# Optimization experiments

Hardware: AMD Instinct MI355X
Metric: run time of the kernel (lower is better)

Reference implementation:

```python
import jax, jax.numpy as jnp
import numpy as np

N = 50000      # nodes
E = 800000     # edges (before self-loops)
IN = 256       # input features
H = 8          # heads
C = 32         # hidden channels per head
OUT = 40       # classes
NEG_SLOPE = 0.2


def setup_inputs() -> dict:
    key = jax.random.key(0)
    ks = jax.random.split(key, 12)
    sd = lambda k, sh: (jax.random.normal(k, sh, jnp.float32) * 0.05)
    return {
        "x": jax.random.normal(ks[0], (N, IN), jnp.float32),
        "edge_index": jax.random.randint(ks[1], (2, E), 0, N),
        "W1": sd(ks[2], (IN, H * C)),
        "a_src1": sd(ks[3], (H, C)),
        "a_dst1": sd(ks[4], (H, C)),
        "b1": jnp.zeros((C,), jnp.float32),
        "W2": sd(ks[5], (C, H * C)),
        "a_src2": sd(ks[6], (H, C)),
        "a_dst2": sd(ks[7], (H, C)),
        "b2": jnp.zeros((C,), jnp.float32),
        "Wo": sd(ks[8], (C, OUT)),
        "bo": jnp.zeros((OUT,), jnp.float32),
    }


def gat_layer(x, src, dst, n, W, a_src, a_dst, b):
    # x: [N, F]; src/dst: [E'] (self-loops included). concat=False -> mean over heads.
    h = (x @ W).reshape(n, H, C)                       # [N, H, C]
    alpha_src = jnp.sum(h * a_src, axis=-1)            # [N, H]
    alpha_dst = jnp.sum(h * a_dst, axis=-1)            # [N, H]
    e = alpha_src[src] + alpha_dst[dst]                # [E', H]
    e = jnp.where(e > 0, e, NEG_SLOPE * e)             # leaky_relu
    # segment softmax over incoming edges of each dst node
    m = jax.ops.segment_max(e, dst, num_segments=n)    # [N, H]
    ex = jnp.exp(e - m[dst])                           # [E', H]
    s = jax.ops.segment_sum(ex, dst, num_segments=n)   # [N, H]
    alpha = ex / s[dst]                                # [E', H]
    msg = alpha[:, :, None] * h[src]                   # [E', H, C]
    out = jax.ops.segment_sum(msg, dst, num_segments=n)  # [N, H, C]
    return out.mean(axis=1) + b                        # [N, C]


def reference(x, edge_index, W1, a_src1, a_dst1, b1, W2, a_src2, a_dst2, b2, Wo, bo):
    n = x.shape[0]
    loops = jnp.arange(n, dtype=edge_index.dtype)
    src = jnp.concatenate([edge_index[0], loops])      # add self-loops (PyG default)
    dst = jnp.concatenate([edge_index[1], loops])
    h = gat_layer(x, src, dst, n, W1, a_src1, a_dst1, b1)
    h = jax.nn.elu(h)                                  # dropout skipped (eval)
    h = gat_layer(h, src, dst, n, W2, a_src2, a_dst2, b2)
    h = jax.nn.elu(h)
    logits = h @ Wo + bo
    return jax.nn.log_softmax(logits, axis=1)
```

## Files before the change

kernel.cpp:

```cpp
#include <hip/hip_runtime.h>
#include <math.h>

#define N_NODES 50000
#define N_PAD   50016
#define N_EDGES 800000
#define E_TOT   (N_EDGES + N_NODES)
#define F_IN    256
#define NHEAD   8
#define CH      32
#define HC      256
#define OUT_C   40
#define NEG_SLOPE 0.2f
#define SCAN_BLOCKS ((N_NODES + 255) / 256)
#define G_DEG   ((E_TOT + 255) / 256)
#define G_XCVT  ((N_NODES * F_IN / 8 + 255) / 256)
#define G_WCVT  ((HC * F_IN + 255) / 256)
#define G_WCVT2 ((HC * CH + 255) / 256)

typedef unsigned short u16;
typedef unsigned int   u32;
typedef unsigned char  u8;
typedef __attribute__((ext_vector_type(8))) short bf16x8;
typedef __attribute__((ext_vector_type(4))) float f32x4;
typedef __attribute__((ext_vector_type(2))) float f32x2;

__device__ __forceinline__ u16 f2bf(float f) {
    union { u32 u; float f; } x; x.f = f;
    u32 u = x.u;
    return (u16)((u + 0x7fffu + ((u >> 16) & 1u)) >> 16);
}
__device__ __forceinline__ float bflo(u32 v) {
    union { u32 u; float f; } x; x.u = v << 16; return x.f;
}
__device__ __forceinline__ u8 f2fp8(float f) {
    return (u8)(__builtin_amdgcn_cvt_pk_fp8_f32(f, f, 0, false) & 0xff);
}


__global__ __launch_bounds__(256) void cvt_kernel(const float* __restrict__ x,
        u16* __restrict__ xb, const float* __restrict__ W1, u16* __restrict__ Wt,
        const float* __restrict__ W2, u16* __restrict__ W2t,
        const int* __restrict__ ei, int* __restrict__ deg) {
    int b = blockIdx.x;
    if (b < G_DEG) {
        int j = b * 256 + threadIdx.x;
        if (j >= E_TOT) return;
        int dstn = (j < N_EDGES) ? ei[N_EDGES + j] : (j - N_EDGES);
        atomicAdd(&deg[dstn], 1);
    } else if (b < G_DEG + G_XCVT) {
        int t = (b - G_DEG) * 256 + threadIdx.x;
        if (t >= N_NODES * F_IN / 8) return;
        const float4* xp = (const float4*)x + (size_t)t * 2;
        float4 v0 = xp[0], v1 = xp[1];
        uint4 o;
        o.x = (u32)f2bf(v0.x) | ((u32)f2bf(v0.y) << 16);
        o.y = (u32)f2bf(v0.z) | ((u32)f2bf(v0.w) << 16);
        o.z = (u32)f2bf(v1.x) | ((u32)f2bf(v1.y) << 16);
        o.w = (u32)f2bf(v1.z) | ((u32)f2bf(v1.w) << 16);
        ((uint4*)xb)[t] = o;
    } else if (b < G_DEG + G_XCVT + G_WCVT) {
        int t = (b - G_DEG - G_XCVT) * 256 + threadIdx.x;
        int n = t & 255, k = t >> 8;
        Wt[(size_t)n * F_IN + k] = f2bf(W1[(size_t)k * HC + n]);
    } else {
        int t = (b - G_DEG - G_XCVT - G_WCVT) * 256 + threadIdx.x;
        if (t >= HC * CH) return;
        int n = t & 255, k = t >> 8;
        W2t[(size_t)n * CH + k] = f2bf(W2[(size_t)k * HC + n]);
    }
}

__global__ __launch_bounds__(256) void gemm1_mfma(const u16* __restrict__ xb,
        const u16* __restrict__ Wt, u8* __restrict__ ht8) {
    const int row0 = blockIdx.x * 32;
    const int t    = threadIdx.x;
    const int wave = t >> 6;
    const int lane = t & 63;
    const int l16  = lane & 15;
    const int quad = lane >> 4;
    const int nb   = wave * 64;

    f32x4 acc[2][4];
    #pragma unroll
    for (int m = 0; m < 2; ++m)
        #pragma unroll
        for (int n = 0; n < 4; ++n) acc[m][n] = (f32x4){0.f, 0.f, 0.f, 0.f};

    const u16* a0p = xb + (size_t)(row0 + l16) * F_IN;
    const u16* a1p = a0p + 16 * F_IN;
    const u16* bp  = Wt + (size_t)(nb + l16) * F_IN;

    #pragma unroll 1
    for (int k0 = 0; k0 < F_IN; k0 += 32) {
        const int ko = k0 + quad * 8;
        bf16x8 a0 = *(const bf16x8*)(a0p + ko);
        bf16x8 a1 = *(const bf16x8*)(a1p + ko);
        bf16x8 b0 = *(const bf16x8*)(bp + 0 * 16 * F_IN + ko);
        bf16x8 b1 = *(const bf16x8*)(bp + 1 * 16 * F_IN + ko);
        bf16x8 b2 = *(const bf16x8*)(bp + 2 * 16 * F_IN + ko);
        bf16x8 b3 = *(const bf16x8*)(bp + 3 * 16 * F_IN + ko);
        acc[0][0] = __builtin_amdgcn_mfma_f32_16x16x32_bf16(a0, b0, acc[0][0], 0, 0, 0);
        acc[0][1] = __builtin_amdgcn_mfma_f32_16x16x32_bf16(a0, b1, acc[0][1], 0, 0, 0);
        acc[0][2] = __builtin_amdgcn_mfma_f32_16x16x32_bf16(a0, b2, acc[0][2], 0, 0, 0);
        acc[0][3] = __builtin_amdgcn_mfma_f32_16x16x32_bf16(a0, b3, acc[0][3], 0, 0, 0);
        acc[1][0] = __builtin_amdgcn_mfma_f32_16x16x32_bf16(a1, b0, acc[1][0], 0, 0, 0);
        acc[1][1] = __builtin_amdgcn_mfma_f32_16x16x32_bf16(a1, b1, acc[1][1], 0, 0, 0);
        acc[1][2] = __builtin_amdgcn_mfma_f32_16x16x32_bf16(a1, b2, acc[1][2], 0, 0, 0);
        acc[1][3] = __builtin_amdgcn_mfma_f32_16x16x32_bf16(a1, b3, acc[1][3], 0, 0, 0);
    }

    #pragma unroll
    for (int m = 0; m < 2; ++m) {
        #pragma unroll
        for (int r = 0; r < 4; ++r) {
            int row = row0 + m * 16 + quad * 4 + r;
            if (row < N_NODES) {
                u8* hr = ht8 + (size_t)row * HC;
                #pragma unroll
                for (int n = 0; n < 4; ++n) {
                    int col = nb + n * 16 + l16;
                    hr[col] = f2fp8(acc[m][n][r]);
                }
            }
        }
    }
}

__global__ __launch_bounds__(256) void gemm2_mfma(const u16* __restrict__ hmb,
        const u16* __restrict__ W2t, u8* __restrict__ ht8) {
    const int row0 = blockIdx.x * 32;
    const int t    = threadIdx.x;
    const int wave = t >> 6;
    const int lane = t & 63;
    const int l16  = lane & 15;
    const int quad = lane >> 4;
    const int nb   = wave * 64;
    const int ko   = quad * 8;

    const u16* a0p = hmb + (size_t)(row0 + l16) * CH;
    const u16* a1p = a0p + 16 * CH;
    const u16* bp  = W2t + (size_t)(nb + l16) * CH;

    bf16x8 a0 = *(const bf16x8*)(a0p + ko);
    bf16x8 a1 = *(const bf16x8*)(a1p + ko);
    bf16x8 b0 = *(const bf16x8*)(bp + 0 * 16 * CH + ko);
    bf16x8 b1 = *(const bf16x8*)(bp + 1 * 16 * CH + ko);
    bf16x8 b2 = *(const bf16x8*)(bp + 2 * 16 * CH + ko);
    bf16x8 b3 = *(const bf16x8*)(bp + 3 * 16 * CH + ko);

    f32x4 z = (f32x4){0.f, 0.f, 0.f, 0.f};
    f32x4 acc[2][4];
    acc[0][0] = __builtin_amdgcn_mfma_f32_16x16x32_bf16(a0, b0, z, 0, 0, 0);
    acc[0][1] = __builtin_amdgcn_mfma_f32_16x16x32_bf16(a0, b1, z, 0, 0, 0);
    acc[0][2] = __builtin_amdgcn_mfma_f32_16x16x32_bf16(a0, b2, z, 0, 0, 0);
    acc[0][3] = __builtin_amdgcn_mfma_f32_16x16x32_bf16(a0, b3, z, 0, 0, 0);
    acc[1][0] = __builtin_amdgcn_mfma_f32_16x16x32_bf16(a1, b0, z, 0, 0, 0);
    acc[1][1] = __builtin_amdgcn_mfma_f32_16x16x32_bf16(a1, b1, z, 0, 0, 0);
    acc[1][2] = __builtin_amdgcn_mfma_f32_16x16x32_bf16(a1, b2, z, 0, 0, 0);
    acc[1][3] = __builtin_amdgcn_mfma_f32_16x16x32_bf16(a1, b3, z, 0, 0, 0);

    #pragma unroll
    for (int m = 0; m < 2; ++m) {
        #pragma unroll
        for (int r = 0; r < 4; ++r) {
            int row = row0 + m * 16 + quad * 4 + r;
            if (row < N_NODES) {
                u8* hr = ht8 + (size_t)row * HC;
                #pragma unroll
                for (int n = 0; n < 4; ++n) {
                    int col = nb + n * 16 + l16;
                    hr[col] = f2fp8(acc[m][n][r]);
                }
            }
        }
    }
}

__global__ __launch_bounds__(256) void alpha_t_kernel(const u8* __restrict__ ht8,
        const float* __restrict__ a_src, const float* __restrict__ a_dst,
        float* __restrict__ asrc, float* __restrict__ adst) {
    __shared__ float sas[HC], sad[HC];
    for (int i = threadIdx.x; i < HC; i += 256) {
        sas[i] = a_src[i];
        sad[i] = a_dst[i];
    }
    __syncthreads();
    int node = blockIdx.x * 256 + threadIdx.x;
    if (node >= N_NODES) return;
    const uint2* hp = (const uint2*)(ht8 + (size_t)node * HC);
    float s1[NHEAD], s2[NHEAD];
    #pragma unroll
    for (int h = 0; h < NHEAD; ++h) {
        float t1 = 0.f, t2 = 0.f;
        #pragma unroll
        for (int i = 0; i < 4; ++i) {
            uint2 v = hp[h * 4 + i];
            f32x2 p01 = __builtin_amdgcn_cvt_pk_f32_fp8(v.x, false);
            f32x2 p23 = __builtin_amdgcn_cvt_pk_f32_fp8(v.x, true);
            f32x2 p45 = __builtin_amdgcn_cvt_pk_f32_fp8(v.y, false);
            f32x2 p67 = __builtin_amdgcn_cvt_pk_f32_fp8(v.y, true);
            const float* s1p = &sas[h * CH + i * 8];
            const float* s2p = &sad[h * CH + i * 8];
            t1 += p01.x * s1p[0] + p01.y * s1p[1] + p23.x * s1p[2] + p23.y * s1p[3]
                + p45.x * s1p[4] + p45.y * s1p[5] + p67.x * s1p[6] + p67.y * s1p[7];
            t2 += p01.x * s2p[0] + p01.y * s2p[1] + p23.x * s2p[2] + p23.y * s2p[3]
                + p45.x * s2p[4] + p45.y * s2p[5] + p67.x * s2p[6] + p67.y * s2p[7];
        }
        s1[h] = t1; s2[h] = t2;
    }
    float4* o1 = (float4*)(asrc + (size_t)node * NHEAD);
    float4* o2 = (float4*)(adst + (size_t)node * NHEAD);
    o1[0] = make_float4(s1[0], s1[1], s1[2], s1[3]);
    o1[1] = make_float4(s1[4], s1[5], s1[6], s1[7]);
    o2[0] = make_float4(s2[0], s2[1], s2[2], s2[3]);
    o2[1] = make_float4(s2[4], s2[5], s2[6], s2[7]);
}

__device__ __forceinline__ int wave_incl_scan(int v, int lane) {
    #pragma unroll
    for (int d = 1; d < 64; d <<= 1) {
        int u = __shfl_up(v, d, 64);
        if (lane >= d) v += u;
    }
    return v;
}

__global__ __launch_bounds__(256) void scan1_kernel(const int* __restrict__ deg,
        int* __restrict__ rowptr, int* __restrict__ partials) {
    const int t    = blockIdx.x * 256 + threadIdx.x;
    const int lane = threadIdx.x & 63;
    const int wid  = threadIdx.x >> 6;
    int v = (t < N_NODES) ? deg[t] : 0;
    int inc = wave_incl_scan(v, lane);
    __shared__ int wtot[4];
    if (lane == 63) wtot[wid] = inc;
    __syncthreads();
    int woff = 0;
    #pragma unroll
    for (int i = 0; i < 4; ++i) woff += (i < wid) ? wtot[i] : 0;
    if (t < N_NODES) rowptr[t] = inc - v + woff;
    if (threadIdx.x == 255) partials[blockIdx.x] = woff + inc;
}

__global__ __launch_bounds__(256) void scan2_kernel(int* __restrict__ partials) {
    const int t    = threadIdx.x;
    const int lane = t & 63;
    const int wid  = t >> 6;
    int v = (t < SCAN_BLOCKS) ? partials[t] : 0;
    int inc = wave_incl_scan(v, lane);
    __shared__ int wtot[4];
    if (lane == 63) wtot[wid] = inc;
    __syncthreads();
    int woff = 0;
    #pragma unroll
    for (int i = 0; i < 4; ++i) woff += (i < wid) ? wtot[i] : 0;
    __syncthreads();
    if (t < SCAN_BLOCKS) partials[t] = inc - v + woff;
}

__global__ __launch_bounds__(256) void scan3_kernel(int* __restrict__ rowptr,
        int* __restrict__ cursor, const int* __restrict__ partials) {
    const int t = blockIdx.x * 256 + threadIdx.x;
    if (t < N_NODES) {
        int v = rowptr[t] + partials[blockIdx.x];
        rowptr[t] = v;
        cursor[t] = v;
    } else if (t == N_NODES) {
        rowptr[N_NODES] = E_TOT;
    }
}

__global__ __launch_bounds__(256) void scatter_kernel(const int* __restrict__ ei,
        int* __restrict__ cursor, u16* __restrict__ csr_src) {
    int j = blockIdx.x * 256 + threadIdx.x;
    if (j >= E_TOT) return;
    int src, dst;
    if (j < N_EDGES) { src = ei[j]; dst = ei[N_EDGES + j]; }
    else             { src = j - N_EDGES; dst = src; }
    int pos = atomicAdd(&cursor[dst], 1);
    csr_src[pos] = (u16)src;
}

__global__ __launch_bounds__(256) void attn_kernel(const int* __restrict__ rowptr,
        const u16* __restrict__ csr_src, const float* __restrict__ asrc,
        const float* __restrict__ adst, const u8* __restrict__ ht8,
        const float* __restrict__ b, u16* __restrict__ out) {
    const int wid = (blockIdx.x * 256 + threadIdx.x) >> 6;
    if (wid >= N_NODES) return;
    const int dst  = wid;
    const int lane = threadIdx.x & 63;
    const int q    = lane >> 4;
    const int l16  = lane & 15;
    const int h    = l16 >> 1;
    const float ad_own = adst[dst * NHEAD + h];
    const u8* hbase = ht8 + l16 * 16;

    f32x2 acc2[8];
    #pragma unroll
    for (int i = 0; i < 8; ++i) acc2[i] = (f32x2){0.f, 0.f};
    float wsum = 0.f;

    const int p0 = rowptr[dst], p1 = rowptr[dst + 1];
    const int nt = (p1 - p0 + 7) >> 3;

    float asA = -1e30f, asB = -1e30f;
    uint4 hvA = make_uint4(0u, 0u, 0u, 0u), hvB = make_uint4(0u, 0u, 0u, 0u);
    int e = p0 + q;
    if (e < p1) {
        int s = (int)csr_src[e];
        asA = asrc[s * NHEAD + h];
        hvA = *(const uint4*)(hbase + ((size_t)s << 8));
    }
    if (e + 4 < p1) {
        int s = (int)csr_src[e + 4];
        asB = asrc[s * NHEAD + h];
        hvB = *(const uint4*)(hbase + ((size_t)s << 8));
    }

    for (int it = 0; it < nt; ++it) {
        float aA = asA; uint4 hA = hvA;
        float aB = asB; uint4 hB = hvB;
        asA = -1e30f; asB = -1e30f;
        if (e + 8 < p1) {
            int s = (int)csr_src[e + 8];
            asA = asrc[s * NHEAD + h];
            hvA = *(const uint4*)(hbase + ((size_t)s << 8));
        }
        if (e + 12 < p1) {
            int s = (int)csr_src[e + 12];
            asB = asrc[s * NHEAD + h];
            hvB = *(const uint4*)(hbase + ((size_t)s << 8));
        }
        {
            float x = aA + ad_own;
            x = x > 0.f ? x : NEG_SLOPE * x;
            float w = __expf(x);
            wsum += w;
            f32x2 w2; w2.x = w; w2.y = w;
            acc2[0] = __builtin_elementwise_fma(w2, __builtin_amdgcn_cvt_pk_f32_fp8(hA.x, false), acc2[0]);
            acc2[1] = __builtin_elementwise_fma(w2, __builtin_amdgcn_cvt_pk_f32_fp8(hA.x, true ), acc2[1]);
            acc2[2] = __builtin_elementwise_fma(w2, __builtin_amdgcn_cvt_pk_f32_fp8(hA.y, false), acc2[2]);
            acc2[3] = __builtin_elementwise_fma(w2, __builtin_amdgcn_cvt_pk_f32_fp8(hA.y, true ), acc2[3]);
            acc2[4] = __builtin_elementwise_fma(w2, __builtin_amdgcn_cvt_pk_f32_fp8(hA.z, false), acc2[4]);
            acc2[5] = __builtin_elementwise_fma(w2, __builtin_amdgcn_cvt_pk_f32_fp8(hA.z, true ), acc2[5]);
            acc2[6] = __builtin_elementwise_fma(w2, __builtin_amdgcn_cvt_pk_f32_fp8(hA.w, false), acc2[6]);
            acc2[7] = __builtin_elementwise_fma(w2, __builtin_amdgcn_cvt_pk_f32_fp8(hA.w, true ), acc2[7]);
        }
        {
            float x = aB + ad_own;
            x = x > 0.f ? x : NEG_SLOPE * x;
            float w = __expf(x);
            wsum += w;
            f32x2 w2; w2.x = w; w2.y = w;
            acc2[0] = __builtin_elementwise_fma(w2, __builtin_amdgcn_cvt_pk_f32_fp8(hB.x, false), acc2[0]);
            acc2[1] = __builtin_elementwise_fma(w2, __builtin_amdgcn_cvt_pk_f32_fp8(hB.x, true ), acc2[1]);
            acc2[2] = __builtin_elementwise_fma(w2, __builtin_amdgcn_cvt_pk_f32_fp8(hB.y, false), acc2[2]);
            acc2[3] = __builtin_elementwise_fma(w2, __builtin_amdgcn_cvt_pk_f32_fp8(hB.y, true ), acc2[3]);
            acc2[4] = __builtin_elementwise_fma(w2, __builtin_amdgcn_cvt_pk_f32_fp8(hB.z, false), acc2[4]);
            acc2[5] = __builtin_elementwise_fma(w2, __builtin_amdgcn_cvt_pk_f32_fp8(hB.z, true ), acc2[5]);
            acc2[6] = __builtin_elementwise_fma(w2, __builtin_amdgcn_cvt_pk_f32_fp8(hB.w, false), acc2[6]);
            acc2[7] = __builtin_elementwise_fma(w2, __builtin_amdgcn_cvt_pk_f32_fp8(hB.w, true ), acc2[7]);
        }
        e += 8;
    }

    #pragma unroll
    for (int i = 0; i < 8; ++i) {
        acc2[i].x += __shfl_xor(acc2[i].x, 16, 64);
        acc2[i].y += __shfl_xor(acc2[i].y, 16, 64);
        acc2[i].x += __shfl_xor(acc2[i].x, 32, 64);
        acc2[i].y += __shfl_xor(acc2[i].y, 32, 64);
    }
    wsum += __shfl_xor(wsum, 16, 64);
    wsum += __shfl_xor(wsum, 32, 64);

    float winv = 1.0f / wsum;
    f32x2 winv2; winv2.x = winv; winv2.y = winv;
    #pragma unroll
    for (int i = 0; i < 8; ++i) acc2[i] *= winv2;

    #pragma unroll
    for (int i = 0; i < 8; ++i) {
        acc2[i].x += __shfl_xor(acc2[i].x, 2, 64);
        acc2[i].y += __shfl_xor(acc2[i].y, 2, 64);
        acc2[i].x += __shfl_xor(acc2[i].x, 4, 64);
        acc2[i].y += __shfl_xor(acc2[i].y, 4, 64);
        acc2[i].x += __shfl_xor(acc2[i].x, 8, 64);
        acc2[i].y += __shfl_xor(acc2[i].y, 8, 64);
    }

    if (lane < 2) {
        const int c0 = lane * 16;
        const float4* bp4 = (const float4*)(b + c0);
        float4 b0 = bp4[0], b1 = bp4[1], b2 = bp4[2], b3 = bp4[3];
        float bb[16] = {b0.x, b0.y, b0.z, b0.w, b1.x, b1.y, b1.z, b1.w,
                        b2.x, b2.y, b2.z, b2.w, b3.x, b3.y, b3.z, b3.w};
        u32 d[8];
        #pragma unroll
        for (int i = 0; i < 8; ++i) {
            float v0 = acc2[i].x * 0.125f + bb[2 * i];
            float v1 = acc2[i].y * 0.125f + bb[2 * i + 1];
            v0 = v0 > 0.f ? v0 : (__expf(v0) - 1.f);
            v1 = v1 > 0.f ? v1 : (__expf(v1) - 1.f);
            d[i] = (u32)f2bf(v0) | ((u32)f2bf(v1) << 16);
        }
        uint4* op = (uint4*)(out + (size_t)dst * CH + c0);
        op[0] = make_uint4(d[0], d[1], d[2], d[3]);
        op[1] = make_uint4(d[4], d[5], d[6], d[7]);
    }
}

__global__ __launch_bounds__(256) void out_kernel(const u16* __restrict__ hf,
        const float* __restrict__ Wo, const float* __restrict__ bo,
        float* __restrict__ out) {
    const int wave = threadIdx.x >> 6;
    const int lane = threadIdx.x & 63;
    const int n    = blockIdx.x * 4 + wave;
    __shared__ float hs[4][CH];
    if (n < N_NODES && lane < CH) hs[wave][lane] = bflo((u32)hf[n * CH + lane]);
    __syncthreads();
    if (n >= N_NODES) return;
    float logit = -INFINITY;
    if (lane < OUT_C) {
        float a = bo[lane];
        #pragma unroll
        for (int k = 0; k < CH; ++k) a += hs[wave][k] * Wo[k * OUT_C + lane];
        logit = a;
    }
    float m = logit;
    #pragma unroll
    for (int off = 32; off; off >>= 1) m = fmaxf(m, __shfl_xor(m, off, 64));
    float ex = (lane < OUT_C) ? __expf(logit - m) : 0.f;
    float ssum = ex;
    #pragma unroll
    for (int off = 32; off; off >>= 1) ssum += __shfl_xor(ssum, off, 64);
    if (lane < OUT_C) out[(size_t)n * OUT_C + lane] = logit - m - __logf(ssum);
}

extern "C" void kernel_launch(void* const* d_in, const int* in_sizes, int n_in,
                              void* d_out, int out_size, void* d_ws, size_t ws_size,
                              hipStream_t stream) {
    const float* x      = (const float*)d_in[0];
    const int*   ei     = (const int*)  d_in[1];
    const float* W1     = (const float*)d_in[2];
    const float* a_src1 = (const float*)d_in[3];
    const float* a_dst1 = (const float*)d_in[4];
    const float* b1     = (const float*)d_in[5];
    const float* W2     = (const float*)d_in[6];
    const float* a_src2 = (const float*)d_in[7];
    const float* a_dst2 = (const float*)d_in[8];
    const float* b2     = (const float*)d_in[9];
    const float* Wo     = (const float*)d_in[10];
    const float* bo     = (const float*)d_in[11];
    float* out = (float*)d_out;

    char* ws = (char*)d_ws;
    size_t off = 0;
    auto carve = [&](size_t bytes) { char* p = ws + off; off += (bytes + 255) & ~(size_t)255; return p; };
    u8*    ht8     = (u8*)   carve((size_t)N_NODES * HC);
    u16*   xb      = (u16*)  carve((size_t)N_PAD * F_IN * 2);
    u16*   Wt      = (u16*)  carve((size_t)HC * F_IN * 2);
    u16*   W2t     = (u16*)  carve((size_t)HC * CH * 2);
    float* asrc    = (float*)carve((size_t)N_NODES * NHEAD * 4);
    float* adst    = (float*)carve((size_t)N_NODES * NHEAD * 4);
    u16*   hmid    = (u16*)  carve((size_t)N_PAD * CH * 2);
    u16*   hout    = (u16*)  carve((size_t)N_NODES * CH * 2);
    int*   deg     = (int*)  carve((size_t)N_NODES * 4);
    int*   rowptr  = (int*)  carve((size_t)(N_NODES + 1) * 4);
    int*   cursor  = (int*)  carve((size_t)N_NODES * 4);
    u16*   csr_src = (u16*)  carve((size_t)E_TOT * 2);
    int*   partials= (int*)  carve((size_t)SCAN_BLOCKS * 4);

    const int g_cvt   = G_DEG + G_XCVT + G_WCVT + G_WCVT2;
    const int g_gemm  = (N_NODES + 31) / 32;
    const int g_node  = (N_NODES + 255) / 256;
    const int g_edge  = (E_TOT + 255) / 256;
    const int g_attn  = (N_NODES * 64 + 255) / 256;
    const int g_out   = (N_NODES + 3) / 4;

    (void)hipMemsetAsync(deg, 0, (size_t)N_NODES * 4, stream);
    cvt_kernel<<<g_cvt, 256, 0, stream>>>(x, xb, W1, Wt, W2, W2t, ei, deg);
    scan1_kernel<<<SCAN_BLOCKS, 256, 0, stream>>>(deg, rowptr, partials);
    scan2_kernel<<<1, 256, 0, stream>>>(partials);
    scan3_kernel<<<SCAN_BLOCKS, 256, 0, stream>>>(rowptr, cursor, partials);
    scatter_kernel<<<g_edge, 256, 0, stream>>>(ei, cursor, csr_src);

    gemm1_mfma<<<g_gemm, 256, 0, stream>>>(xb, Wt, ht8);
    alpha_t_kernel<<<g_node, 256, 0, stream>>>(ht8, a_src1, a_dst1, asrc, adst);
    attn_kernel<<<g_attn, 256, 0, stream>>>(rowptr, csr_src, asrc, adst, ht8, b1, hmid);

    gemm2_mfma<<<g_gemm, 256, 0, stream>>>(hmid, W2t, ht8);
    alpha_t_kernel<<<g_node, 256, 0, stream>>>(ht8, a_src2, a_dst2, asrc, adst);
    attn_kernel<<<g_attn, 256, 0, stream>>>(rowptr, csr_src, asrc, adst, ht8, b2, hout);

    out_kernel<<<g_out, 256, 0, stream>>>(hout, Wo, bo, out);
}
```

Baseline: 383.0 us.

## Fuse x bf16 conversion into GEMM1 and range-partition degree/scatter atomics

GEMM1 now reads fp32 x directly and packs it to bf16 in registers, removing the separate x conversion pass and its bf16 intermediate buffer. The degree count and CSR scatter are restructured so that each block handles a chunk of edges but only performs atomics for destinations in one of eight node ranges, localizing atomic traffic to improve cache locality. The cost is that each edge index is read eight times and GEMM1 loads twice as many bytes for the A operand, with the conversion repeated for every column block.

```diff
diff --git a/kernel.cpp b/kernel.cpp
--- a/kernel.cpp
+++ b/kernel.cpp
@@ -12,10 +12,12 @@
 #define OUT_C   40
 #define NEG_SLOPE 0.2f
 #define SCAN_BLOCKS ((N_NODES + 255) / 256)
-#define G_DEG   ((E_TOT + 255) / 256)
-#define G_XCVT  ((N_NODES * F_IN / 8 + 255) / 256)
 #define G_WCVT  ((HC * F_IN + 255) / 256)
 #define G_WCVT2 ((HC * CH + 255) / 256)
+#define NRANGE  8
+#define RANGE_SZ (N_NODES / NRANGE)
+#define BIN_CHUNK 2048
+#define G_BINCH ((E_TOT + BIN_CHUNK - 1) / BIN_CHUNK)
 
 typedef unsigned short u16;
 typedef unsigned int   u32;
@@ -35,42 +37,32 @@
 __device__ __forceinline__ u8 f2fp8(float f) {
     return (u8)(__builtin_amdgcn_cvt_pk_fp8_f32(f, f, 0, false) & 0xff);
 }
-
-
-__global__ __launch_bounds__(256) void cvt_kernel(const float* __restrict__ x,
-        u16* __restrict__ xb, const float* __restrict__ W1, u16* __restrict__ Wt,
-        const float* __restrict__ W2, u16* __restrict__ W2t,
-        const int* __restrict__ ei, int* __restrict__ deg) {
+__device__ __forceinline__ bf16x8 pack_bf16x8(float4 a, float4 b) {
+    bf16x8 r;
+    r[0] = (short)f2bf(a.x); r[1] = (short)f2bf(a.y);
+    r[2] = (short)f2bf(a.z); r[3] = (short)f2bf(a.w);
+    r[4] = (short)f2bf(b.x); r[5] = (short)f2bf(b.y);
+    r[6] = (short)f2bf(b.z); r[7] = (short)f2bf(b.w);
+    return r;
+}
+
+
+__global__ __launch_bounds__(256) void cvt_kernel(const float* __restrict__ W1,
+        u16* __restrict__ Wt, const float* __restrict__ W2, u16* __restrict__ W2t) {
     int b = blockIdx.x;
-    if (b < G_DEG) {
-        int j = b * 256 + threadIdx.x;
-        if (j >= E_TOT) return;
-        int dstn = (j < N_EDGES) ? ei[N_EDGES + j] : (j - N_EDGES);
-        atomicAdd(&deg[dstn], 1);
-    } else if (b < G_DEG + G_XCVT) {
-        int t = (b - G_DEG) * 256 + threadIdx.x;
-        if (t >= N_NODES * F_IN / 8) return;
-        const float4* xp = (const float4*)x + (size_t)t * 2;
-        float4 v0 = xp[0], v1 = xp[1];
-        uint4 o;
-        o.x = (u32)f2bf(v0.x) | ((u32)f2bf(v0.y) << 16);
-        o.y = (u32)f2bf(v0.z) | ((u32)f2bf(v0.w) << 16);
-        o.z = (u32)f2bf(v1.x) | ((u32)f2bf(v1.y) << 16);
-        o.w = (u32)f2bf(v1.z) | ((u32)f2bf(v1.w) << 16);
-        ((uint4*)xb)[t] = o;
-    } else if (b < G_DEG + G_XCVT + G_WCVT) {
-        int t = (b - G_DEG - G_XCVT) * 256 + threadIdx.x;
+    if (b < G_WCVT) {
+        int t = b * 256 + threadIdx.x;
         int n = t & 255, k = t >> 8;
         Wt[(size_t)n * F_IN + k] = f2bf(W1[(size_t)k * HC + n]);
     } else {
-        int t = (b - G_DEG - G_XCVT - G_WCVT) * 256 + threadIdx.x;
+        int t = (b - G_WCVT) * 256 + threadIdx.x;
         if (t >= HC * CH) return;
         int n = t & 255, k = t >> 8;
         W2t[(size_t)n * CH + k] = f2bf(W2[(size_t)k * HC + n]);
     }
 }
 
-__global__ __launch_bounds__(256) void gemm1_mfma(const u16* __restrict__ xb,
+__global__ __launch_bounds__(256) void gemm1_mfma(const float* __restrict__ x,
         const u16* __restrict__ Wt, u8* __restrict__ ht8) {
     const int row0 = blockIdx.x * 32;
     const int t    = threadIdx.x;
@@ -86,15 +78,21 @@
         #pragma unroll
         for (int n = 0; n < 4; ++n) acc[m][n] = (f32x4){0.f, 0.f, 0.f, 0.f};
 
-    const u16* a0p = xb + (size_t)(row0 + l16) * F_IN;
-    const u16* a1p = a0p + 16 * F_IN;
-    const u16* bp  = Wt + (size_t)(nb + l16) * F_IN;
+    const int ar0 = min(row0 + l16, N_NODES - 1);
+    const int ar1 = min(row0 + 16 + l16, N_NODES - 1);
+    const float* a0p = x + (size_t)ar0 * F_IN;
+    const float* a1p = x + (size_t)ar1 * F_IN;
+    const u16*   bp  = Wt + (size_t)(nb + l16) * F_IN;
 
     #pragma unroll 1
     for (int k0 = 0; k0 < F_IN; k0 += 32) {
         const int ko = k0 + quad * 8;
-        bf16x8 a0 = *(const bf16x8*)(a0p + ko);
-        bf16x8 a1 = *(const bf16x8*)(a1p + ko);
+        float4 a0lo = *(const float4*)(a0p + ko);
+        float4 a0hi = *(const float4*)(a0p + ko + 4);
+        float4 a1lo = *(const float4*)(a1p + ko);
+        float4 a1hi = *(const float4*)(a1p + ko + 4);
+        bf16x8 a0 = pack_bf16x8(a0lo, a0hi);
+        bf16x8 a1 = pack_bf16x8(a1lo, a1hi);
         bf16x8 b0 = *(const bf16x8*)(bp + 0 * 16 * F_IN + ko);
         bf16x8 b1 = *(const bf16x8*)(bp + 1 * 16 * F_IN + ko);
         bf16x8 b2 = *(const bf16x8*)(bp + 2 * 16 * F_IN + ko);
@@ -216,6 +214,22 @@
     o2[1] = make_float4(s2[4], s2[5], s2[6], s2[7]);
 }
 
+__global__ __launch_bounds__(256) void deg_kernel(const int* __restrict__ ei,
+        int* __restrict__ deg) {
+    const int r  = blockIdx.x & (NRANGE - 1);
+    const int ch = blockIdx.x >> 3;
+    const int lo = r * RANGE_SZ, hi = lo + RANGE_SZ;
+    int j0 = ch * BIN_CHUNK + threadIdx.x;
+    #pragma unroll
+    for (int i = 0; i < BIN_CHUNK / 256; ++i) {
+        int j = j0 + i * 256;
+        if (j < E_TOT) {
+            int d = (j < N_EDGES) ? ei[N_EDGES + j] : (j - N_EDGES);
+            if (d >= lo && d < hi) atomicAdd(&deg[d], 1);
+        }
+    }
+}
+
 __device__ __forceinline__ int wave_incl_scan(int v, int lane) {
     #pragma unroll
     for (int d = 1; d < 64; d <<= 1) {
@@ -272,13 +286,22 @@
 
 __global__ __launch_bounds__(256) void scatter_kernel(const int* __restrict__ ei,
         int* __restrict__ cursor, u16* __restrict__ csr_src) {
-    int j = blockIdx.x * 256 + threadIdx.x;
-    if (j >= E_TOT) return;
-    int src, dst;
-    if (j < N_EDGES) { src = ei[j]; dst = ei[N_EDGES + j]; }
-    else             { src = j - N_EDGES; dst = src; }
-    int pos = atomicAdd(&cursor[dst], 1);
-    csr_src[pos] = (u16)src;
+    const int r  = blockIdx.x & (NRANGE - 1);
+    const int ch = blockIdx.x >> 3;
+    const int lo = r * RANGE_SZ, hi = lo + RANGE_SZ;
+    int j0 = ch * BIN_CHUNK + threadIdx.x;
+    #pragma unroll
+    for (int i = 0; i < BIN_CHUNK / 256; ++i) {
+        int j = j0 + i * 256;
+        if (j < E_TOT) {
+            int d = (j < N_EDGES) ? ei[N_EDGES + j] : (j - N_EDGES);
+            if (d >= lo && d < hi) {
+                int s = (j < N_EDGES) ? ei[j] : d;
+                int pos = atomicAdd(&cursor[d], 1);
+                csr_src[pos] = (u16)s;
+            }
+        }
+    }
 }
 
 __global__ __launch_bounds__(256) void attn_kernel(const int* __restrict__ rowptr,
@@ -458,7 +481,6 @@
     size_t off = 0;
     auto carve = [&](size_t bytes) { char* p = ws + off; off += (bytes + 255) & ~(size_t)255; return p; };
     u8*    ht8     = (u8*)   carve((size_t)N_NODES * HC);
-    u16*   xb      = (u16*)  carve((size_t)N_PAD * F_IN * 2);
     u16*   Wt      = (u16*)  carve((size_t)HC * F_IN * 2);
     u16*   W2t     = (u16*)  carve((size_t)HC * CH * 2);
     float* asrc    = (float*)carve((size_t)N_NODES * NHEAD * 4);
@@ -471,21 +493,22 @@
     u16*   csr_src = (u16*)  carve((size_t)E_TOT * 2);
     int*   partials= (int*)  carve((size_t)SCAN_BLOCKS * 4);
 
-    const int g_cvt   = G_DEG + G_XCVT + G_WCVT + G_WCVT2;
+    const int g_cvt   = G_WCVT + G_WCVT2;
+    const int g_bin   = G_BINCH * NRANGE;
     const int g_gemm  = (N_NODES + 31) / 32;
     const int g_node  = (N_NODES + 255) / 256;
-    const int g_edge  = (E_TOT + 255) / 256;
     const int g_attn  = (N_NODES * 64 + 255) / 256;
     const int g_out   = (N_NODES + 3) / 4;
 
     (void)hipMemsetAsync(deg, 0, (size_t)N_NODES * 4, stream);
-    cvt_kernel<<<g_cvt, 256, 0, stream>>>(x, xb, W1, Wt, W2, W2t, ei, deg);
+    cvt_kernel<<<g_cvt, 256, 0, stream>>>(W1, Wt, W2, W2t);
+    deg_kernel<<<g_bin, 256, 0, stream>>>(ei, deg);
     scan1_kernel<<<SCAN_BLOCKS, 256, 0, stream>>>(deg, rowptr, partials);
     scan2_kernel<<<1, 256, 0, stream>>>(partials);
     scan3_kernel<<<SCAN_BLOCKS, 256, 0, stream>>>(rowptr, cursor, partials);
-    scatter_kernel<<<g_edge, 256, 0, stream>>>(ei, cursor, csr_src);
-
-    gemm1_mfma<<<g_gemm, 256, 0, stream>>>(xb, Wt, ht8);
+    scatter_kernel<<<g_bin, 256, 0, stream>>>(ei, cursor, csr_src);
+
+    gemm1_mfma<<<g_gemm, 256, 0, stream>>>(x, Wt, ht8);
     alpha_t_kernel<<<g_node, 256, 0, stream>>>(ht8, a_src1, a_dst1, asrc, adst);
     attn_kernel<<<g_attn, 256, 0, stream>>>(rowptr, csr_src, asrc, adst, ht8, b1, hmid);
 
```

After: 387.9 us. Within noise of the previous version (+1.3%).
